# Optimization experiments

Hardware: AMD Instinct MI355X
Metric: run time of the kernel (lower is better)

Reference implementation:

```python
import jax, jax.numpy as jnp
import numpy as np

SCALE = 32.0      # backbone feature->image coordinate scale (stride)
LOG_EPS = 1e-8    # geometry.safe_log epsilon


def _safe_log(x):
    return jnp.log(jnp.maximum(x, LOG_EPS))


def setup_inputs() -> dict:
    key = jax.random.key(0)
    k1, k2, k3, k4, k5, k6 = jax.random.split(key, 6)
    B, P, L = 128, 4096, 128
    cls_scores = jax.random.normal(k1, (B, 2 * P), dtype=jnp.float32)
    bbox_deltas = jax.random.normal(k2, (B, 4 * P), dtype=jnp.float32) * 0.1
    # RoI in feature coordinates: x,y in [0,40), w,h in [1,11)
    roi_xy = jax.random.uniform(k3, (B, P, 2), dtype=jnp.float32) * 40.0
    roi_wh = jax.random.uniform(k4, (B, P, 2), dtype=jnp.float32) * 10.0 + 1.0
    roi = jnp.concatenate([roi_xy, roi_wh], axis=-1)
    # Ground-truth labels in image coordinates: x,y in [0,1280), w,h in [32,352)
    lab_xy = jax.random.uniform(k5, (B, L, 2), dtype=jnp.float32) * 1280.0
    lab_wh = jax.random.uniform(k6, (B, L, 2), dtype=jnp.float32) * 320.0 + 32.0
    labels = jnp.concatenate([lab_xy, lab_wh], axis=-1)
    return {
        "cls_scores": cls_scores,
        "bbox_deltas": bbox_deltas,
        "roi": roi,
        "labels": labels,
        "neg_enabled": 1,
    }


def reference(cls_scores, bbox_deltas, roi, labels, neg_enabled):
    """Vectorized port of ClassifierModel._compute_loss summed over the batch.

    cls_scores  [B, 2P] laid out [class, proposal] (cls[i::P] -> per-proposal logits)
    bbox_deltas [B, 4P] laid out [coord, proposal]
    roi         [B, P, 4] proposals in feature coords (x,y,w,h)
    labels      [B, L, 4] ground-truth boxes in image coords (x,y,w,h)
    """
    B, P = roi.shape[0], roi.shape[1]
    roi_img = roi.astype(jnp.float32) * SCALE  # feature -> image coords

    # --- IoU matrix [B, L, P] (geometry.calculate_IoU over all label/proposal pairs)
    l = labels[:, :, None, :]   # [B, L, 1, 4]
    r = roi_img[:, None, :, :]  # [B, 1, P, 4]
    ix = jnp.maximum(0.0, jnp.minimum(l[..., 0] + l[..., 2], r[..., 0] + r[..., 2]) - jnp.maximum(l[..., 0], r[..., 0]))
    iy = jnp.maximum(0.0, jnp.minimum(l[..., 1] + l[..., 3], r[..., 1] + r[..., 3]) - jnp.maximum(l[..., 1], r[..., 1]))
    inter = ix * iy
    union = l[..., 2] * l[..., 3] + r[..., 2] * r[..., 3] - inter
    iou = jnp.where(union > 0.0, inter / union, 0.0)  # [B, L, P]

    # --- matching: argmax over labels where any IoU is nonzero, else -1
    any_hit = jnp.sum((iou != 0.0).astype(jnp.int32), axis=1) > 0        # [B, P]
    match = jnp.where(any_hit, jnp.argmax(iou, axis=1), -1)              # [B, P]
    pos = match > 0  # NOTE: original uses match[i] > 0 (strict), kept faithfully

    matched = jnp.take_along_axis(labels, jnp.clip(match, 0)[:, :, None], axis=1)  # [B, P, 4]
    tx = (matched[..., 0] - roi_img[..., 0]) / roi_img[..., 2]
    ty = (matched[..., 1] - roi_img[..., 1]) / roi_img[..., 3]
    tw = _safe_log(matched[..., 2] / roi_img[..., 2])
    th = _safe_log(matched[..., 3] / roi_img[..., 3])
    targets = jnp.stack([tx, ty, tw, th], axis=-1)                        # [B, P, 4]
    preds = bbox_deltas.reshape(B, 4, P).transpose(0, 2, 1)               # [B, P, 4]

    # Huber (delta=1, mean over the 4 coords) per proposal
    err = targets - preds
    ae = jnp.abs(err)
    huber = jnp.mean(jnp.where(ae <= 1.0, 0.5 * err * err, ae - 0.5), axis=-1)  # [B, P]

    # --- classification: softmax over the two per-proposal logits, then
    # CategoricalCrossentropy(probs, const) = -sum(probs * log(const))
    logits = cls_scores.reshape(B, 2, P).transpose(0, 2, 1)               # [B, P, 2]
    probs = jax.nn.softmax(logits, axis=-1)
    log_pos = jnp.log(jnp.array([0.1, 0.9], dtype=jnp.float32))
    log_neg = jnp.log(jnp.array([0.9, 0.1], dtype=jnp.float32))
    ce_pos = -jnp.sum(probs * log_pos, axis=-1)                           # [B, P]
    ce_neg = -jnp.sum(probs * log_neg, axis=-1)                           # [B, P]

    neg_term = jnp.where(jnp.asarray(neg_enabled) > 0, ce_neg, 0.0)
    per_prop = jnp.where(pos, 2.0 * huber + ce_pos, neg_term)             # [B, P]
    return jnp.sum(per_prop)
```

## Files before the change

kernel.cpp:

```cpp
#include <hip/hip_runtime.h>
#include <hip/hip_bf16.h>
#include <math.h>

#define BB 128
#define PP 4096
#define LL 128
#define BLOCK 256
#define PROPS 2
#define CHUNKS (PP / (BLOCK * PROPS))
#define SCALE 32.0f

__global__ __launch_bounds__(BLOCK) void classifier_loss_kernel(
    const float* __restrict__ cls,
    const float* __restrict__ bbox,
    const float* __restrict__ roi,
    const float* __restrict__ labels,
    const int* __restrict__ neg_enabled,
    float* __restrict__ out)
{
    __shared__ float s_red[BLOCK / 64];

    const int b     = blockIdx.x >> 3;
    const int chunk = blockIdx.x & (CHUNKS - 1);
    const int pbase = chunk * (BLOCK * PROPS) + threadIdx.x;

    const float* __restrict__ lab = labels + (size_t)b * LL * 4;

    float rx[PROPS], ry[PROPS], rx2[PROPS], ry2[PROPS], rarea[PROPS];
    float bi[PROPS], bd[PROPS];
    int   bidx[PROPS];

    #pragma unroll
    for (int j = 0; j < PROPS; ++j) {
        const int p = pbase + j * BLOCK;
        const float* rp = roi + ((size_t)b * PP + p) * 4;
        rx[j]  = rp[0] * SCALE;
        ry[j]  = rp[1] * SCALE;
        float rw = rp[2] * SCALE, rh = rp[3] * SCALE;
        rx2[j] = rx[j] + rw;
        ry2[j] = ry[j] + rh;
        rarea[j] = rw * rh;
        bi[j] = -1.0f;
        bd[j] = 1.0f;
        bidx[j] = 0;
    }

    #pragma unroll 4
    for (int li = 0; li < LL; ++li) {
        const float lx = lab[li * 4 + 0];
        const float ly = lab[li * 4 + 1];
        const float lw = lab[li * 4 + 2];
        const float lh = lab[li * 4 + 3];
        const float x2 = lx + lw;
        const float y2 = ly + lh;
        const float area = lw * lh;
        #pragma unroll
        for (int j = 0; j < PROPS; ++j) {
            float ix = fmaxf(0.0f, fminf(x2, rx2[j]) - fmaxf(lx, rx[j]));
            float iy = fmaxf(0.0f, fminf(y2, ry2[j]) - fmaxf(ly, ry[j]));
            float inter = ix * iy;
            float denom = area + rarea[j];
            bool gt = inter * bd[j] > bi[j] * denom;
            bi[j]   = gt ? inter : bi[j];
            bd[j]   = gt ? denom : bd[j];
            bidx[j] = gt ? li    : bidx[j];
        }
    }

    const float LOG01 = -2.3025850929940457f;
    const float LOG09 = -0.10536051565782628f;
    const bool neg_on = neg_enabled[0] > 0;

    float acc = 0.0f;
    #pragma unroll
    for (int j = 0; j < PROPS; ++j) {
        const int p = pbase + j * BLOCK;
        const bool pos = (bi[j] > 0.0f) && (bidx[j] > 0);

        const float s0 = cls[(size_t)b * 2 * PP + p];
        const float s1 = cls[(size_t)b * 2 * PP + PP + p];
        const float mx = fmaxf(s0, s1);
        const float e0 = expf(s0 - mx);
        const float e1 = expf(s1 - mx);
        const float inv = 1.0f / (e0 + e1);
        const float p0 = e0 * inv, p1 = e1 * inv;
        const float ce_pos = -(p0 * LOG01 + p1 * LOG09);
        const float ce_neg = -(p0 * LOG09 + p1 * LOG01);

        float per;
        if (pos) {
            const float* mp = lab + bidx[j] * 4;
            float mxl = mp[0], myl = mp[1], mwl = mp[2], mhl = mp[3];
            float rw = rx2[j] - rx[j];
            float rh = ry2[j] - ry[j];
            float tx = (mxl - rx[j]) / rw;
            float ty = (myl - ry[j]) / rh;
            float tw = logf(fmaxf(mwl / rw, 1e-8f));
            float th = logf(fmaxf(mhl / rh, 1e-8f));
            const float* bp = bbox + (size_t)b * 4 * PP + p;
            float ex = tx - bp[0];
            float ey = ty - bp[PP];
            float ew = tw - bp[2 * PP];
            float eh = th - bp[3 * PP];
            float ax = fabsf(ex), ay = fabsf(ey), aw = fabsf(ew), ah = fabsf(eh);
            float hx = (ax <= 1.0f) ? 0.5f * ex * ex : ax - 0.5f;
            float hy = (ay <= 1.0f) ? 0.5f * ey * ey : ay - 0.5f;
            float hw = (aw <= 1.0f) ? 0.5f * ew * ew : aw - 0.5f;
            float hh = (ah <= 1.0f) ? 0.5f * eh * eh : ah - 0.5f;
            float huber = 0.25f * (hx + hy + hw + hh);
            per = 2.0f * huber + ce_pos;
        } else {
            per = neg_on ? ce_neg : 0.0f;
        }
        acc += per;
    }

    float v = acc;
    #pragma unroll
    for (int off = 32; off > 0; off >>= 1)
        v += __shfl_down(v, off, 64);
    if ((threadIdx.x & 63) == 0)
        s_red[threadIdx.x >> 6] = v;
    __syncthreads();
    if (threadIdx.x == 0) {
        float blk = s_red[0] + s_red[1] + s_red[2] + s_red[3];
        atomicAdd(out, blk);
    }
}

extern "C" void kernel_launch(void* const* d_in, const int* in_sizes, int n_in,
                              void* d_out, int out_size, void* d_ws, size_t ws_size,
                              hipStream_t stream) {
    const float* cls    = (const float*)d_in[0];
    const float* bbox   = (const float*)d_in[1];
    const float* roi    = (const float*)d_in[2];
    const float* labels = (const float*)d_in[3];
    const int*   neg    = (const int*)d_in[4];
    float* out = (float*)d_out;

    hipMemsetAsync(out, 0, sizeof(float) * out_size, stream);
    classifier_loss_kernel<<<dim3(BB * CHUNKS), dim3(BLOCK), 0, stream>>>(
        cls, bbox, roi, labels, neg, out);
}
```

Measured before the change: 115.4 us.

## Precompute label box corners and areas in SoA layout via prep kernel

```diff
diff --git a/kernel.cpp b/kernel.cpp
--- a/kernel.cpp
+++ b/kernel.cpp
@@ -9,11 +9,30 @@
 #define PROPS 2
 #define CHUNKS (PP / (BLOCK * PROPS))
 #define SCALE 32.0f
+#define LCHUNK 8
+
+__global__ __launch_bounds__(256) void prep_labels_kernel(
+    const float* __restrict__ labels, float* __restrict__ labp)
+{
+    int i = blockIdx.x * 256 + threadIdx.x;
+    if (i < BB * LL) {
+        int b = i >> 7, li = i & (LL - 1);
+        const float* lp = labels + (size_t)i * 4;
+        float x = lp[0], y = lp[1], w = lp[2], h = lp[3];
+        float* o = labp + (size_t)b * (5 * LL) + li;
+        o[0 * LL] = x;
+        o[1 * LL] = y;
+        o[2 * LL] = x + w;
+        o[3 * LL] = y + h;
+        o[4 * LL] = w * h;
+    }
+}
 
 __global__ __launch_bounds__(BLOCK) void classifier_loss_kernel(
     const float* __restrict__ cls,
     const float* __restrict__ bbox,
     const float* __restrict__ roi,
+    const float* __restrict__ labp,
     const float* __restrict__ labels,
     const int* __restrict__ neg_enabled,
     float* __restrict__ out)
@@ -24,9 +43,10 @@
     const int chunk = blockIdx.x & (CHUNKS - 1);
     const int pbase = chunk * (BLOCK * PROPS) + threadIdx.x;
 
-    const float* __restrict__ lab = labels + (size_t)b * LL * 4;
+    const float* __restrict__ lb = labp + (size_t)b * (5 * LL);
 
     float rx[PROPS], ry[PROPS], rx2[PROPS], ry2[PROPS], rarea[PROPS];
+    float cs0[PROPS], cs1[PROPS];
     float bi[PROPS], bd[PROPS];
     int   bidx[PROPS];
 
@@ -34,9 +54,12 @@
     for (int j = 0; j < PROPS; ++j) {
         const int p = pbase + j * BLOCK;
         const float* rp = roi + ((size_t)b * PP + p) * 4;
-        rx[j]  = rp[0] * SCALE;
-        ry[j]  = rp[1] * SCALE;
-        float rw = rp[2] * SCALE, rh = rp[3] * SCALE;
+        float r0 = rp[0], r1 = rp[1], r2 = rp[2], r3 = rp[3];
+        cs0[j] = cls[(size_t)b * 2 * PP + p];
+        cs1[j] = cls[(size_t)b * 2 * PP + PP + p];
+        rx[j]  = r0 * SCALE;
+        ry[j]  = r1 * SCALE;
+        float rw = r2 * SCALE, rh = r3 * SCALE;
         rx2[j] = rx[j] + rw;
         ry2[j] = ry[j] + rh;
         rarea[j] = rw * rh;
@@ -45,25 +68,26 @@
         bidx[j] = 0;
     }
 
-    #pragma unroll 4
-    for (int li = 0; li < LL; ++li) {
-        const float lx = lab[li * 4 + 0];
-        const float ly = lab[li * 4 + 1];
-        const float lw = lab[li * 4 + 2];
-        const float lh = lab[li * 4 + 3];
-        const float x2 = lx + lw;
-        const float y2 = ly + lh;
-        const float area = lw * lh;
+    for (int lc = 0; lc < LL; lc += LCHUNK) {
         #pragma unroll
-        for (int j = 0; j < PROPS; ++j) {
-            float ix = fmaxf(0.0f, fminf(x2, rx2[j]) - fmaxf(lx, rx[j]));
-            float iy = fmaxf(0.0f, fminf(y2, ry2[j]) - fmaxf(ly, ry[j]));
-            float inter = ix * iy;
-            float denom = area + rarea[j];
-            bool gt = inter * bd[j] > bi[j] * denom;
-            bi[j]   = gt ? inter : bi[j];
-            bd[j]   = gt ? denom : bd[j];
-            bidx[j] = gt ? li    : bidx[j];
+        for (int u = 0; u < LCHUNK; ++u) {
+            const int li = lc + u;
+            const float s_x    = lb[0 * LL + li];
+            const float s_y    = lb[1 * LL + li];
+            const float s_x2   = lb[2 * LL + li];
+            const float s_y2   = lb[3 * LL + li];
+            const float s_area = lb[4 * LL + li];
+            #pragma unroll
+            for (int j = 0; j < PROPS; ++j) {
+                float ix = fmaxf(0.0f, fminf(s_x2, rx2[j]) - fmaxf(s_x, rx[j]));
+                float iy = fmaxf(0.0f, fminf(s_y2, ry2[j]) - fmaxf(s_y, ry[j]));
+                float inter = ix * iy;
+                float denom = s_area + rarea[j];
+                bool gt = inter * bd[j] > bi[j] * denom;
+                bi[j]   = gt ? inter : bi[j];
+                bd[j]   = gt ? denom : bd[j];
+                bidx[j] = gt ? li    : bidx[j];
+            }
         }
     }
 
@@ -77,11 +101,9 @@
         const int p = pbase + j * BLOCK;
         const bool pos = (bi[j] > 0.0f) && (bidx[j] > 0);
 
-        const float s0 = cls[(size_t)b * 2 * PP + p];
-        const float s1 = cls[(size_t)b * 2 * PP + PP + p];
-        const float mx = fmaxf(s0, s1);
-        const float e0 = expf(s0 - mx);
-        const float e1 = expf(s1 - mx);
+        const float mx = fmaxf(cs0[j], cs1[j]);
+        const float e0 = expf(cs0[j] - mx);
+        const float e1 = expf(cs1[j] - mx);
         const float inv = 1.0f / (e0 + e1);
         const float p0 = e0 * inv, p1 = e1 * inv;
         const float ce_pos = -(p0 * LOG01 + p1 * LOG09);
@@ -89,7 +111,7 @@
 
         float per;
         if (pos) {
-            const float* mp = lab + bidx[j] * 4;
+            const float* mp = labels + ((size_t)b * LL + bidx[j]) * 4;
             float mxl = mp[0], myl = mp[1], mwl = mp[2], mhl = mp[3];
             float rw = rx2[j] - rx[j];
             float rh = ry2[j] - ry[j];
@@ -136,9 +158,12 @@
     const float* roi    = (const float*)d_in[2];
     const float* labels = (const float*)d_in[3];
     const int*   neg    = (const int*)d_in[4];
-    float* out = (float*)d_out;
+    float* out  = (float*)d_out;
+    float* labp = (float*)d_ws;
 
     hipMemsetAsync(out, 0, sizeof(float) * out_size, stream);
-    classifier_loss_kernel<<<dim3(BB * CHUNKS), dim3(BLOCK), 0, stream>>>(
-        cls, bbox, roi, labels, neg, out);
+    prep_labels_kernel<<<dim3((BB * LL + 255) / 256), dim3(256), 0, stream>>>(
+        labels, labp);
+    classifier_loss_kernel<<<dim3(BB * PP / (BLOCK * PROPS)), dim3(BLOCK), 0, stream>>>(
+        cls, bbox, roi, labp, labels, neg, out);
 }
```

New measurement: 110.5 us. 4.3% less time.
